# Kernel optimization log

Measured on AMD Instinct MI355X. Metric: run time of the kernel, lower is better.

The kernel has to match this reference:

```python
import jax, jax.numpy as jnp
import numpy as np

jax.config.update("jax_enable_x64", True)

VOCAB_R_MAX = 3.0
EPS = 1e-8


def _sanitize(x):
    # torch.nan_to_num(x, nan=0.0, posinf=10000.0, neginf=-10000.0)
    return jnp.nan_to_num(x, nan=0.0, posinf=10000.0, neginf=-10000.0)


def setup_inputs() -> dict:
    key = jax.random.key(0)
    k1, k2 = jax.random.split(key, 2)
    B, L, V, n = 2, 512, 50257, 768
    hidden_states = jax.random.normal(k1, (B, L, n + 1), dtype=jnp.float32)
    # nn.Parameter(torch.randn(V, n) * 0.01) -- tangent vectors
    weight = jax.random.normal(k2, (V, n), dtype=jnp.float32) * 0.01
    # init_temp = 1/sqrt(n_embd)
    logit_scale = jnp.asarray(1.0 / np.sqrt(n), dtype=jnp.float32)
    return {"hidden_states": hidden_states, "weight": weight, "logit_scale": logit_scale}


def _exp_map_zero(v_spatial, max_tangent_norm):
    # Lorentz exp map at origin (curvature -1), tangent vector (0, v_spatial).
    # Norm is clamped to max_tangent_norm (geodesic radius ceiling).
    r = jnp.linalg.norm(v_spatial, axis=-1, keepdims=True)  # [V,1]
    rc = jnp.minimum(r, max_tangent_norm)
    dirv = v_spatial / jnp.maximum(r, EPS)
    return jnp.concatenate([jnp.cosh(rc), jnp.sinh(rc) * dirv], axis=-1)  # [V, n+1]


def _ensure_lorentz(x):
    # Project onto the hyperboloid: x0 = sqrt(1 + ||x_spatial||^2)
    sp = x[..., 1:]
    t = jnp.sqrt(1.0 + jnp.sum(sp * sp, axis=-1, keepdims=True))
    return jnp.concatenate([t, sp], axis=-1)


def reference(hidden_states, weight, logit_scale):
    x = _ensure_lorentz(_sanitize(hidden_states))          # [B,L,n+1]
    w = _sanitize(_exp_map_zero(weight, VOCAB_R_MAX))       # [V,n+1]

    x64 = x.astype(jnp.float64)
    w64 = w.astype(jnp.float64)
    # Minkowski inner product split into time/space einsums (as in source)
    time_inner = jnp.einsum('blt,vt->blv', x64[..., :1], w64[:, :1])
    space_inner = jnp.einsum('bls,vs->blv', x64[..., 1:], w64[:, 1:])
    inner = space_inner - time_inner                        # [B,L,V] fp64

    tau = jnp.clip(logit_scale, 0.01, 2.5).astype(jnp.float64)
    logits = (inner * tau).astype(hidden_states.dtype)
    return _sanitize(logits)
```

## Files before the change

kernel.cpp:

```cpp
#include <hip/hip_runtime.h>
#include <hip/hip_bf16.h>
#include <cstdint>
#include <cstddef>

typedef __attribute__((ext_vector_type(4))) float f32x4;
typedef __attribute__((ext_vector_type(8))) short bf16x8;
typedef unsigned short ushort_t;

#define KDIM 768
#define GQ 96
#define BM 128
#define BN 256
#define BK 32
#define NKT 24

static __device__ __forceinline__ float sani(float x) {
  if (__builtin_isnan(x)) return 0.0f;
  if (__builtin_isinf(x)) return x > 0.0f ? 1.0e4f : -1.0e4f;
  return x;
}

static __device__ __forceinline__ unsigned short f2bf(float x) {
  unsigned u = __builtin_bit_cast(unsigned, x);
  unsigned r = 0x7FFFu + ((u >> 16) & 1u);
  return (unsigned short)((u + r) >> 16);
}


__global__ __launch_bounds__(256) void prep_x_kernel(
    const float* __restrict__ h, ushort_t* __restrict__ xl,
    float* __restrict__ tx) {
  const int row = blockIdx.x;
  const int t = threadIdx.x;
  const float* src = h + (size_t)row * (KDIM + 1) + 1;
  float v0 = sani(src[t]);
  float v1 = sani(src[t + 256]);
  float v2 = sani(src[t + 512]);
  float ss = v0 * v0 + v1 * v1 + v2 * v2;
#pragma unroll
  for (int off = 32; off > 0; off >>= 1) ss += __shfl_down(ss, off);
  __shared__ float red[4];
  if ((t & 63) == 0) red[t >> 6] = ss;
  __syncthreads();
  if (t == 0) {
    float total = red[0] + red[1] + red[2] + red[3];
    tx[row] = sqrtf(1.0f + total);
  }
  ushort_t* dst = xl + (size_t)row * KDIM;
  dst[t]       = f2bf(v0);
  dst[t + 256] = f2bf(v1);
  dst[t + 512] = f2bf(v2);
}

__global__ __launch_bounds__(256) void prep_w_kernel(
    const float* __restrict__ w, ushort_t* __restrict__ wt,
    float* __restrict__ cw, int V, int Vpad) {
  __shared__ float fs[8 * KDIM];
  __shared__ float redv[8], scs[8];
  const int t = threadIdx.x;
  const int r = t >> 5, j = t & 31;
  const int row = blockIdx.x * 8 + r;
  const bool valid = row < V;
  const float* src = w + (size_t)row * KDIM;
  float ss = 0.0f;
#pragma unroll
  for (int k = 0; k < 24; ++k) {
    float v = valid ? src[j + 32 * k] : 0.0f;
    fs[r * KDIM + j + 32 * k] = v;
    ss = fmaf(v, v, ss);
  }
#pragma unroll
  for (int m = 16; m > 0; m >>= 1) ss += __shfl_xor(ss, m);
  if (j == 0) redv[r] = ss;
  __syncthreads();
  if (t < 8) {
    const int rw = blockIdx.x * 8 + t;
    float rr = sqrtf(redv[t]);
    float rc = fminf(rr, 3.0f);
    float e = expf(rc), ei = 1.0f / e;
    scs[t] = (rw < V) ? 0.5f * (e - ei) / fmaxf(rr, 1e-8f) : 0.0f;
    cw[rw] = (rw < V) ? sani(0.5f * (e + ei)) : 0.0f;
  }
  __syncthreads();
#pragma unroll
  for (int p = 0; p < 3; ++p) {
    const int c = t + 256 * p;
    const int g = c >> 3, rl = c & 7;
    const float sc = scs[rl];
    ushort_t pk[8];
#pragma unroll
    for (int e = 0; e < 8; ++e)
      pk[e] = f2bf(sani(fs[rl * KDIM + g * 8 + e] * sc));
    *(uint4*)&wt[((size_t)g * Vpad + blockIdx.x * 8 + rl) * 8] =
        *(const uint4*)pk;
  }
}

#define GLD16(gp, sp)                                               \
  __builtin_amdgcn_global_load_lds(                                 \
      (const __attribute__((address_space(1))) void*)(gp),          \
      (__attribute__((address_space(3))) void*)(sp), 16, 0, 0)

__global__ __launch_bounds__(256, 2) void gemm_kernel(
    const ushort_t* __restrict__ xl, const ushort_t* __restrict__ wt,
    const float* __restrict__ tx, const float* __restrict__ cw,
    const float* __restrict__ ls, float* __restrict__ out,
    int V, int Vpad, int nwg8) {
  __shared__ ushort_t lds[3 * 4096];

  const int tid = threadIdx.x;
  const int lane = tid & 63;
  const int wid = tid >> 6;
  const int l15 = lane & 15;
  const int lq = lane >> 4;

  const int g = blockIdx.x;
  const int L = (g & 7) * nwg8 + (g >> 3);
  const int bm = L & 7;
  const int bn = L >> 3;

  const int a_row0 = bm * BM;
  const int b_row0 = bn * BN + wid * 64;

  const int ggl = (lane & 7) ^ (lane >> 3);
  const int rl = 2 * (lane >> 3) + (ggl >> 2);
  const int cg = (ggl & 3) * 8;
  const ushort_t* pA0 = xl + (size_t)(a_row0 + 16 * wid + rl) * KDIM + cg;
  const ushort_t* pA1 = xl + (size_t)(a_row0 + 16 * (wid + 4) + rl) * KDIM + cg;

  const int rphys = l15 >> 1;
  const int gph = (((l15 & 1) << 2) + lq) ^ rphys;
  const int aoff = rphys * 64 + gph * 8;

  const ushort_t* bp = wt + ((size_t)lq * Vpad + b_row0 + l15) * 8;
  const size_t BSTEP = (size_t)4 * Vpad * 8;

  f32x4 acc[8][4];
#pragma unroll
  for (int i = 0; i < 8; ++i)
#pragma unroll
    for (int j = 0; j < 4; ++j) acc[i][j] = (f32x4){0.f, 0.f, 0.f, 0.f};

  bf16x8 afA[8], afB[8], bfA[4], bfB[4];

#define LOADB(T_, D_)                                                         \
  {                                                                           \
    const ushort_t* p_ = bp + (size_t)(T_) * BSTEP;                           \
    D_[0] = *(const bf16x8*)(p_);                                             \
    D_[1] = *(const bf16x8*)(p_ + 128);                                       \
    D_[2] = *(const bf16x8*)(p_ + 256);                                       \
    D_[3] = *(const bf16x8*)(p_ + 384);                                       \
  }

#define STAGE_A(T_, S_)                                                       \
  {                                                                           \
    GLD16(pA0 + (T_) * BK, &lds[(S_) * 4096 + wid * 512]);                    \
    GLD16(pA1 + (T_) * BK, &lds[(S_) * 4096 + (wid + 4) * 512]);              \
  }

#define READS_A(S_, D_)                                                       \
  _Pragma("unroll") for (int mi = 0; mi < 8; ++mi)                            \
      D_[mi] = *(const bf16x8*)&lds[(S_) * 4096 + mi * 512 + aoff];

#define MFMA32(AF_, BF_)                                                      \
  __builtin_amdgcn_s_setprio(1);                                              \
  _Pragma("unroll") for (int mi = 0; mi < 8; ++mi)                            \
    _Pragma("unroll") for (int ni = 0; ni < 4; ++ni)                          \
        acc[mi][ni] = __builtin_amdgcn_mfma_f32_16x16x32_bf16(                \
            BF_[ni], AF_[mi], acc[mi][ni], 0, 0, 0);                          \
  __builtin_amdgcn_s_setprio(0);

#define SBAR __builtin_amdgcn_sched_barrier(0)
#define BAR __builtin_amdgcn_s_barrier()

#define BODY(T_, S1_, S2_, CA_, CB_, NA_, NB_)                                \
  {                                                                           \
    LOADB((T_) + 1, NB_);                                                     \
    SBAR;                                                                     \
    STAGE_A((T_) + 2, S2_);                                                   \
    SBAR;                                                                     \
    asm volatile("s_waitcnt vmcnt(6)" ::: "memory");                          \
    BAR;                                                                      \
    READS_A(S1_, NA_);                                                        \
    SBAR;                                                                     \
    asm volatile("s_waitcnt lgkmcnt(8)" ::: "memory");                        \
    SBAR;                                                                     \
    MFMA32(CA_, CB_);                                                         \
    BAR;                                                                      \
  }

  LOADB(0, bfA);
  SBAR;
  STAGE_A(0, 0);
  STAGE_A(1, 1);
  SBAR;
  asm volatile("s_waitcnt vmcnt(2)" ::: "memory");
  BAR;
  READS_A(0, afA);

#define GROUP(T0_)                                                            \
  BODY((T0_) + 0, 1, 2, afA, bfA, afB, bfB);                                  \
  BODY((T0_) + 1, 2, 0, afB, bfB, afA, bfA);                                  \
  BODY((T0_) + 2, 0, 1, afA, bfA, afB, bfB);                                  \
  BODY((T0_) + 3, 1, 2, afB, bfB, afA, bfA);                                  \
  BODY((T0_) + 4, 2, 0, afA, bfA, afB, bfB);                                  \
  BODY((T0_) + 5, 0, 1, afB, bfB, afA, bfA);

  GROUP(0)
  GROUP(6)
  GROUP(12)
  BODY(18, 1, 2, afA, bfA, afB, bfB);
  BODY(19, 2, 0, afB, bfB, afA, bfA);
  BODY(20, 0, 1, afA, bfA, afB, bfB);
  BODY(21, 1, 2, afB, bfB, afA, bfA);
  LOADB(23, bfB);
  SBAR;
  asm volatile("s_waitcnt vmcnt(4)" ::: "memory");
  BAR;
  READS_A(2, afB);
  SBAR;
  asm volatile("s_waitcnt lgkmcnt(8)" ::: "memory");
  SBAR;
  MFMA32(afA, bfA);
  BAR;
  asm volatile("s_waitcnt vmcnt(0) lgkmcnt(0)" ::: "memory");
  SBAR;
  MFMA32(afB, bfB);

  float tau = ls[0];
  tau = fminf(fmaxf(tau, 0.01f), 2.5f);

#pragma unroll
  for (int mi = 0; mi < 8; ++mi) {
    const int mg = a_row0 + mi * 16 + l15;
    const float txm = tx[mg];
    float* orow = out + (size_t)mg * V;
#pragma unroll
    for (int ni = 0; ni < 4; ++ni) {
      const int nb = b_row0 + ni * 16 + lq * 4;
      const f32x4 cw4 = *(const f32x4*)&cw[nb];
      f32x4 v;
#pragma unroll
      for (int j = 0; j < 4; ++j)
        v[j] = (acc[mi][ni][j] - txm * cw4[j]) * tau;
      if (nb + 3 < V) {
        __builtin_memcpy(&orow[nb], &v, 16);
      } else {
#pragma unroll
        for (int j = 0; j < 4; ++j)
          if (nb + j < V) orow[nb + j] = v[j];
      }
    }
  }
#undef LOADB
#undef STAGE_A
#undef READS_A
#undef MFMA32
#undef BODY
#undef GROUP
#undef SBAR
#undef BAR
}

extern "C" void kernel_launch(void* const* d_in, const int* in_sizes, int n_in,
                              void* d_out, int out_size, void* d_ws, size_t ws_size,
                              hipStream_t stream) {
  const float* h = (const float*)d_in[0];
  const float* w = (const float*)d_in[1];
  const float* ls = (const float*)d_in[2];
  float* out = (float*)d_out;

  const int M = in_sizes[0] / (KDIM + 1);
  const int V = in_sizes[1] / KDIM;
  const int Vpad = (V + BN - 1) & ~(BN - 1);

  char* ws = (char*)d_ws;
  ushort_t* wt = (ushort_t*)ws;
  ushort_t* xl = (ushort_t*)(ws + (size_t)GQ * Vpad * 8 * 2);
  float* cw = (float*)(ws + (size_t)GQ * Vpad * 8 * 2 + (size_t)M * KDIM * 2);
  float* tx = cw + Vpad;

  prep_x_kernel<<<dim3(M), dim3(256), 0, stream>>>(h, xl, tx);
  prep_w_kernel<<<dim3(Vpad / 8), dim3(256), 0, stream>>>(w, wt, cw, V, Vpad);

  const int nwg = (M / BM) * (Vpad / BN);
  gemm_kernel<<<dim3(nwg), dim3(256), 0, stream>>>(
      xl, wt, tx, cw, ls, out, V, Vpad, nwg / 8);
}
```

Measured before the change: 214.8 us.

## Shrink GEMM tiles to 64x64 single-wave workgroups with double-buffered LDS

Replaces the 128x256 tile, four-wave workgroup and its triple-buffered, barrier-synchronised pipeline with 64x64 tiles, one wave per workgroup and a simple double-buffered loop with no barriers. The aim is to cut synchronisation overhead and raise occupancy and the number of workgroups, which should help balance the output-write-bound epilogue. In exchange, each weight tile is re-read by twice as many row blocks and there is less register-level reuse per MFMA, which increases L2 and memory traffic.

```diff
diff --git a/kernel.cpp b/kernel.cpp
--- a/kernel.cpp
+++ b/kernel.cpp
@@ -9,8 +9,8 @@
 
 #define KDIM 768
 #define GQ 96
-#define BM 128
-#define BN 256
+#define BM 64
+#define BN 64
 #define BK 32
 #define NKT 24
 
@@ -101,32 +101,32 @@
       (const __attribute__((address_space(1))) void*)(gp),          \
       (__attribute__((address_space(3))) void*)(sp), 16, 0, 0)
 
-__global__ __launch_bounds__(256, 2) void gemm_kernel(
+__global__ __launch_bounds__(64, 4) void gemm_kernel(
     const ushort_t* __restrict__ xl, const ushort_t* __restrict__ wt,
     const float* __restrict__ tx, const float* __restrict__ cw,
     const float* __restrict__ ls, float* __restrict__ out,
     int V, int Vpad, int nwg8) {
-  __shared__ ushort_t lds[3 * 4096];
-
-  const int tid = threadIdx.x;
-  const int lane = tid & 63;
-  const int wid = tid >> 6;
+  __shared__ ushort_t lds[2 * 2048];
+
+  const int lane = threadIdx.x;
   const int l15 = lane & 15;
   const int lq = lane >> 4;
 
   const int g = blockIdx.x;
   const int L = (g & 7) * nwg8 + (g >> 3);
-  const int bm = L & 7;
-  const int bn = L >> 3;
+  const int bm = L & 15;
+  const int bn = L >> 4;
 
   const int a_row0 = bm * BM;
-  const int b_row0 = bn * BN + wid * 64;
+  const int b_row0 = bn * BN;
 
   const int ggl = (lane & 7) ^ (lane >> 3);
   const int rl = 2 * (lane >> 3) + (ggl >> 2);
   const int cg = (ggl & 3) * 8;
-  const ushort_t* pA0 = xl + (size_t)(a_row0 + 16 * wid + rl) * KDIM + cg;
-  const ushort_t* pA1 = xl + (size_t)(a_row0 + 16 * (wid + 4) + rl) * KDIM + cg;
+  const ushort_t* pc0 = xl + (size_t)(a_row0 + 0  + rl) * KDIM + cg;
+  const ushort_t* pc1 = xl + (size_t)(a_row0 + 16 + rl) * KDIM + cg;
+  const ushort_t* pc2 = xl + (size_t)(a_row0 + 32 + rl) * KDIM + cg;
+  const ushort_t* pc3 = xl + (size_t)(a_row0 + 48 + rl) * KDIM + cg;
 
   const int rphys = l15 >> 1;
   const int gph = (((l15 & 1) << 2) + lq) ^ rphys;
@@ -135,13 +135,21 @@
   const ushort_t* bp = wt + ((size_t)lq * Vpad + b_row0 + l15) * 8;
   const size_t BSTEP = (size_t)4 * Vpad * 8;
 
-  f32x4 acc[8][4];
-#pragma unroll
-  for (int i = 0; i < 8; ++i)
+  f32x4 acc[4][4];
+#pragma unroll
+  for (int i = 0; i < 4; ++i)
 #pragma unroll
     for (int j = 0; j < 4; ++j) acc[i][j] = (f32x4){0.f, 0.f, 0.f, 0.f};
 
-  bf16x8 afA[8], afB[8], bfA[4], bfB[4];
+  bf16x8 af[4], bfA[4], bfB[4];
+
+#define STAGE_A(T_, S_)                                                       \
+  {                                                                           \
+    GLD16(pc0 + (T_) * BK, &lds[(S_) * 2048 + 0 * 512]);                      \
+    GLD16(pc1 + (T_) * BK, &lds[(S_) * 2048 + 1 * 512]);                      \
+    GLD16(pc2 + (T_) * BK, &lds[(S_) * 2048 + 2 * 512]);                      \
+    GLD16(pc3 + (T_) * BK, &lds[(S_) * 2048 + 3 * 512]);                      \
+  }
 
 #define LOADB(T_, D_)                                                         \
   {                                                                           \
@@ -152,86 +160,44 @@
     D_[3] = *(const bf16x8*)(p_ + 384);                                       \
   }
 
-#define STAGE_A(T_, S_)                                                       \
-  {                                                                           \
-    GLD16(pA0 + (T_) * BK, &lds[(S_) * 4096 + wid * 512]);                    \
-    GLD16(pA1 + (T_) * BK, &lds[(S_) * 4096 + (wid + 4) * 512]);              \
-  }
-
-#define READS_A(S_, D_)                                                       \
-  _Pragma("unroll") for (int mi = 0; mi < 8; ++mi)                            \
-      D_[mi] = *(const bf16x8*)&lds[(S_) * 4096 + mi * 512 + aoff];
-
-#define MFMA32(AF_, BF_)                                                      \
-  __builtin_amdgcn_s_setprio(1);                                              \
-  _Pragma("unroll") for (int mi = 0; mi < 8; ++mi)                            \
+#define READ_A(S_)                                                            \
+  _Pragma("unroll") for (int mi = 0; mi < 4; ++mi)                            \
+      af[mi] = *(const bf16x8*)&lds[(S_) * 2048 + mi * 512 + aoff];
+
+#define MFMA16(CB_)                                                           \
+  _Pragma("unroll") for (int mi = 0; mi < 4; ++mi)                            \
     _Pragma("unroll") for (int ni = 0; ni < 4; ++ni)                          \
         acc[mi][ni] = __builtin_amdgcn_mfma_f32_16x16x32_bf16(                \
-            BF_[ni], AF_[mi], acc[mi][ni], 0, 0, 0);                          \
-  __builtin_amdgcn_s_setprio(0);
-
-#define SBAR __builtin_amdgcn_sched_barrier(0)
-#define BAR __builtin_amdgcn_s_barrier()
-
-#define BODY(T_, S1_, S2_, CA_, CB_, NA_, NB_)                                \
+            CB_[ni], af[mi], acc[mi][ni], 0, 0, 0);
+
+#define ITER(T_, S_, CB_, NB_)                                                \
   {                                                                           \
+    STAGE_A((T_) + 1, (S_) ^ 1);                                              \
     LOADB((T_) + 1, NB_);                                                     \
-    SBAR;                                                                     \
-    STAGE_A((T_) + 2, S2_);                                                   \
-    SBAR;                                                                     \
-    asm volatile("s_waitcnt vmcnt(6)" ::: "memory");                          \
-    BAR;                                                                      \
-    READS_A(S1_, NA_);                                                        \
-    SBAR;                                                                     \
-    asm volatile("s_waitcnt lgkmcnt(8)" ::: "memory");                        \
-    SBAR;                                                                     \
-    MFMA32(CA_, CB_);                                                         \
-    BAR;                                                                      \
-  }
-
+    asm volatile("s_waitcnt vmcnt(8)" ::: "memory");                          \
+    READ_A(S_);                                                               \
+    MFMA16(CB_);                                                              \
+  }
+
+  STAGE_A(0, 0);
   LOADB(0, bfA);
-  SBAR;
-  STAGE_A(0, 0);
-  STAGE_A(1, 1);
-  SBAR;
-  asm volatile("s_waitcnt vmcnt(2)" ::: "memory");
-  BAR;
-  READS_A(0, afA);
-
-#define GROUP(T0_)                                                            \
-  BODY((T0_) + 0, 1, 2, afA, bfA, afB, bfB);                                  \
-  BODY((T0_) + 1, 2, 0, afB, bfB, afA, bfA);                                  \
-  BODY((T0_) + 2, 0, 1, afA, bfA, afB, bfB);                                  \
-  BODY((T0_) + 3, 1, 2, afB, bfB, afA, bfA);                                  \
-  BODY((T0_) + 4, 2, 0, afA, bfA, afB, bfB);                                  \
-  BODY((T0_) + 5, 0, 1, afB, bfB, afA, bfA);
-
-  GROUP(0)
-  GROUP(6)
-  GROUP(12)
-  BODY(18, 1, 2, afA, bfA, afB, bfB);
-  BODY(19, 2, 0, afB, bfB, afA, bfA);
-  BODY(20, 0, 1, afA, bfA, afB, bfB);
-  BODY(21, 1, 2, afB, bfB, afA, bfA);
-  LOADB(23, bfB);
-  SBAR;
-  asm volatile("s_waitcnt vmcnt(4)" ::: "memory");
-  BAR;
-  READS_A(2, afB);
-  SBAR;
-  asm volatile("s_waitcnt lgkmcnt(8)" ::: "memory");
-  SBAR;
-  MFMA32(afA, bfA);
-  BAR;
-  asm volatile("s_waitcnt vmcnt(0) lgkmcnt(0)" ::: "memory");
-  SBAR;
-  MFMA32(afB, bfB);
+
+#pragma unroll 1
+  for (int tt = 0; tt < 11; ++tt) {
+    const int t0 = 2 * tt;
+    ITER(t0, 0, bfA, bfB);
+    ITER(t0 + 1, 1, bfB, bfA);
+  }
+  ITER(22, 0, bfA, bfB);
+  asm volatile("s_waitcnt vmcnt(0)" ::: "memory");
+  READ_A(1);
+  MFMA16(bfB);
 
   float tau = ls[0];
   tau = fminf(fmaxf(tau, 0.01f), 2.5f);
 
 #pragma unroll
-  for (int mi = 0; mi < 8; ++mi) {
+  for (int mi = 0; mi < 4; ++mi) {
     const int mg = a_row0 + mi * 16 + l15;
     const float txm = tx[mg];
     float* orow = out + (size_t)mg * V;
@@ -252,14 +218,11 @@
       }
     }
   }
+#undef STAGE_A
 #undef LOADB
-#undef STAGE_A
-#undef READS_A
-#undef MFMA32
-#undef BODY
-#undef GROUP
-#undef SBAR
-#undef BAR
+#undef READ_A
+#undef MFMA16
+#undef ITER
 }
 
 extern "C" void kernel_launch(void* const* d_in, const int* in_sizes, int n_in,
@@ -284,6 +247,6 @@
   prep_w_kernel<<<dim3(Vpad / 8), dim3(256), 0, stream>>>(w, wt, cw, V, Vpad);
 
   const int nwg = (M / BM) * (Vpad / BN);
-  gemm_kernel<<<dim3(nwg), dim3(256), 0, stream>>>(
+  gemm_kernel<<<dim3(nwg), dim3(64), 0, stream>>>(
       xl, wt, tx, cw, ls, out, V, Vpad, nwg / 8);
 }
```

Result: slower. 247.0 us (+15.0%).
